# Optimization experiments

Hardware: AMD Instinct MI355X
Metric: run time of the kernel (lower is better)

Reference implementation:

```python
import jax, jax.numpy as jnp
import numpy as np
import math

N, B, S = 2048, 4, 1024
SFZ, IFZ, H, A = 384, 256, 8, 64
LN_EPS = 1e-5


def setup_inputs() -> dict:
    key = jax.random.key(0)
    ks = jax.random.split(key, 12)
    x = jax.random.normal(ks[0], (N, IFZ), dtype=jnp.float32)
    emb = jax.random.normal(ks[1], (B, S, SFZ), dtype=jnp.float32)
    mask = jax.random.randint(ks[2], (B, S), 0, 2).astype(bool)
    batch = jnp.sort(jax.random.randint(ks[3], (N,), 0, B)).astype(jnp.int64)
    sc = 1.0 / math.sqrt(IFZ)
    scs = 1.0 / math.sqrt(SFZ)
    Wq = jax.random.normal(ks[4], (IFZ, H * A), dtype=jnp.float32) * sc
    Wk = jax.random.normal(ks[5], (SFZ, H * A), dtype=jnp.float32) * scs
    Wv = jax.random.normal(ks[6], (SFZ, H * A), dtype=jnp.float32) * scs
    Wg = jax.random.normal(ks[7], (IFZ, H * A), dtype=jnp.float32) * sc
    bg = jnp.zeros((H * A,), dtype=jnp.float32)
    Wback = jax.random.normal(ks[8], (H * A, IFZ), dtype=jnp.float32) / math.sqrt(H * A)
    bback = jnp.zeros((IFZ,), dtype=jnp.float32)
    gamma = jnp.ones((IFZ,), dtype=jnp.float32)
    beta = jnp.zeros((IFZ,), dtype=jnp.float32)
    return {"x": x, "packed_sequence_emb": emb, "packed_sequence_mask": mask,
            "batch": batch, "Wq": Wq, "Wk": Wk, "Wv": Wv, "Wg": Wg, "bg": bg,
            "Wback": Wback, "bback": bback, "gamma": gamma, "beta": beta}


def _masked_softmax(scores, mask):
    # scores: [N,S,H], mask: [N,S,1] bool; softmax over S with padded entries zeroed
    neg = jnp.finfo(scores.dtype).min
    s = jnp.where(mask, scores, neg)
    s = s - jnp.max(s, axis=1, keepdims=True)
    e = jnp.exp(s) * mask
    return e / (jnp.sum(e, axis=1, keepdims=True) + 1e-9)


def reference(x, packed_sequence_emb, packed_sequence_mask, batch,
              Wq, Wk, Wv, Wg, bg, Wback, bback, gamma, beta):
    scale = math.sqrt(A)
    q = (x @ Wq).reshape(N, H, A)                               # [N,H,A]
    k = (packed_sequence_emb @ Wk).reshape(B, S, H, A)          # [B,S,H,A]
    v = (packed_sequence_emb @ Wv).reshape(B, S, H, A)
    # scores per (node, candidate-batch), then gather node's own batch entry;
    # avoids materializing k[batch] of shape [N,S,H,A]
    scores_all = jnp.einsum('nha,bsha->nbsh', q, k) / scale     # [N,B,S,H]
    idx = batch[:, None, None, None].astype(jnp.int32)
    scores = jnp.take_along_axis(scores_all, idx, axis=1)[:, 0]  # [N,S,H]
    bmask = packed_sequence_mask[batch][..., None]               # [N,S,1]
    w = _masked_softmax(scores, bmask)                           # [N,S,H]
    feat_all = jnp.einsum('nsh,bsha->nbha', w, v)                # [N,B,H,A]
    feat = jnp.take_along_axis(feat_all, idx, axis=1)[:, 0]      # [N,H,A]
    gate = jax.nn.sigmoid(x @ Wg + bg).reshape(N, H, A)
    new = (gate * feat).reshape(N, H * A) @ Wback + bback        # [N,IFZ]
    y = math.sqrt(2.0) * x + new
    mu = jnp.mean(y, axis=-1, keepdims=True)
    var = jnp.mean((y - mu) ** 2, axis=-1, keepdims=True)
    out = (y - mu) * jax.lax.rsqrt(var + LN_EPS) * gamma + beta
    seq_aa_logits = jnp.sum(scores[..., :2], axis=-1)            # [N,S]
    return out, seq_aa_logits
```

## Files before the change

### kernel.cpp

```cpp
#include <hip/hip_runtime.h>
#include <hip/hip_bf16.h>

#define NND 2048
#define BBATCH 4
#define SS 1024
#define SFZ 384
#define IFZ 256
#define HH 8
#define AA 64
#define HA 512
#define NBX 48
#define NSPL 8

typedef __attribute__((ext_vector_type(8))) short bf16x8;
typedef __attribute__((ext_vector_type(4))) float f32x4;
typedef __attribute__((ext_vector_type(2))) unsigned int u32x2;

__device__ __forceinline__ unsigned short f2bf(float f) {
    union { float f; unsigned u; } a; a.f = f;
    unsigned r = a.u + 0x7fffu + ((a.u >> 16) & 1u);
    return (unsigned short)(r >> 16);
}
__device__ __forceinline__ float bf2f(unsigned short u) {
    return __uint_as_float((unsigned)u << 16);
}

__device__ __forceinline__ bf16x8 cvt8(const float* __restrict__ p) {
    const float4 f0 = *(const float4*)p;
    const float4 f1 = *(const float4*)(p + 4);
    bf16x8 o;
    o[0] = (short)f2bf(f0.x); o[1] = (short)f2bf(f0.y);
    o[2] = (short)f2bf(f0.z); o[3] = (short)f2bf(f0.w);
    o[4] = (short)f2bf(f1.x); o[5] = (short)f2bf(f1.y);
    o[6] = (short)f2bf(f1.z); o[7] = (short)f2bf(f1.w);
    return o;
}

__device__ __forceinline__ bf16x8 gld16(const unsigned short* p) {
    bf16x8 r;
    asm volatile("global_load_dwordx4 %0, %1, off" : "=&v"(r) : "v"(p));
    return r;
}
__device__ __forceinline__ f32x4 gldf4(const float* p) {
    f32x4 r;
    asm volatile("global_load_dwordx4 %0, %1, off" : "=&v"(r) : "v"(p));
    return r;
}
__device__ __forceinline__ u32x2 gld8(const unsigned short* p) {
    u32x2 r;
    asm volatile("global_load_dwordx2 %0, %1, off" : "=&v"(r) : "v"(p));
    return r;
}
__device__ __forceinline__ float gldf(const float* p) {
    float r;
    asm volatile("global_load_dword %0, %1, off" : "=&v"(r) : "v"(p));
    return r;
}
#define VMWAIT0() do { \
    asm volatile("s_waitcnt vmcnt(0)" ::: "memory"); \
    __builtin_amdgcn_sched_barrier(0); \
} while (0)

__device__ __forceinline__ void tile_transpose(
    const float* __restrict__ src, unsigned short* __restrict__ dst,
    int K, int N, int kt, int nt, int t)
{
    __shared__ unsigned short tile[64][65];
    const int k0 = kt * 64, n0 = nt * 64;
    const int tr = t >> 6, tc = t & 63;
    #pragma unroll
    for (int r = 0; r < 16; ++r)
        tile[tr + r*4][tc] = f2bf(src[(size_t)(k0 + tr + r*4) * N + n0 + tc]);
    __syncthreads();
    #pragma unroll
    for (int r = 0; r < 16; ++r)
        dst[(size_t)(n0 + tr + r*4) * K + k0 + tc] = tile[tc][tr + r*4];
}

__global__ __launch_bounds__(256) void prep_kernel(
    const float* __restrict__ Wk, const float* __restrict__ Wv,
    const float* __restrict__ Wq, const float* __restrict__ Wg,
    const float* __restrict__ Wback,
    const void* __restrict__ mask_raw, const void* __restrict__ batch_raw,
    unsigned short* __restrict__ WkT, unsigned short* __restrict__ WvT,
    unsigned short* __restrict__ WqT, unsigned short* __restrict__ WgT,
    unsigned short* __restrict__ WbackT,
    float* __restrict__ mask_f, int* __restrict__ seg)
{
    const int bx = blockIdx.x, t = threadIdx.x;
    if (bx < 48)  { tile_transpose(Wk, WkT, SFZ, HA, bx/8, bx%8, t); return; }
    if (bx < 96)  { const int i = bx-48;  tile_transpose(Wv, WvT, SFZ, HA, i/8, i%8, t); return; }
    if (bx < 128) { const int i = bx-96;  tile_transpose(Wq, WqT, IFZ, HA, i/8, i%8, t); return; }
    if (bx < 160) { const int i = bx-128; tile_transpose(Wg, WgT, IFZ, HA, i/8, i%8, t); return; }
    if (bx < 192) { const int i = bx-160; tile_transpose(Wback, WbackT, HA, IFZ, i/4, i%4, t); return; }
    __shared__ int fl[4];
    __shared__ int fb;
    __shared__ int cnt[4];
    if (t < 4) { fl[t] = 0; cnt[t] = 0; }
    if (t == 0) fb = 0;
    __syncthreads();
    const unsigned char*  mb = (const unsigned char*)mask_raw;
    const unsigned short* mh = (const unsigned short*)mask_raw;
    const unsigned int*   mw = (const unsigned int*)mask_raw;
    int f0 = 0, f1 = 0, f2 = 0, f3 = 0;
    for (int i = t; i < 2048; i += 256) {
        unsigned short h = mh[i];
        if (h == 0x3f80u) f0 = 1;
        if ((i & 1) == 0 && h != 0) f1 = 1;
    }
    for (int i = t; i < 4096; i += 256)
        if ((i & 3) != 0 && mb[i] != 0) f2 = 1;
    for (int i = t; i < 1024; i += 256)
        if ((i & 1) != 0 && mw[i] != 0) f3 = 1;
    const int* bw = (const int*)batch_raw;
    int f4 = 0;
    for (int i = t + 1; i < 2048; i += 256)
        if (bw[i] < bw[i-1]) f4 = 1;
    if (f0) atomicOr(&fl[0], 1);
    if (f1) atomicOr(&fl[1], 1);
    if (f2) atomicOr(&fl[2], 1);
    if (f3) atomicOr(&fl[3], 1);
    if (f4) atomicOr(&fb, 1);
    __syncthreads();
    int mode;
    if (fl[0])      mode = fl[1] ? 1 : 0;
    else if (fl[2]) mode = 2;
    else if (fl[3]) mode = 3;
    else            mode = 4;
    for (int s = t; s < BBATCH*SS; s += 256) {
        int m;
        switch (mode) {
            case 0:  m = (mw[s]   != 0); break;
            case 1:  m = (mh[s]   != 0); break;
            case 2:  m = (mb[s]   != 0); break;
            case 3:  m = (mw[s]   != 0); break;
            default: m = (mw[2*s] != 0); break;
        }
        mask_f[s] = m ? 1.0f : 0.0f;
    }
    const int b64 = fb;
    for (int i = t; i < NND; i += 256) {
        const int bv = (b64 ? bw[2*i] : bw[i]) & 3;
        atomicAdd(&cnt[bv], 1);
    }
    __syncthreads();
    if (t == 0) {
        int s = 0;
        for (int b = 0; b < 4; ++b) { seg[2*b] = s; s += cnt[b]; seg[2*b+1] = s; }
    }
}

__global__ __launch_bounds__(256, 2) void proj_mfma(
    const float* __restrict__ emb, const float* __restrict__ x,
    const unsigned short* __restrict__ WkT, const unsigned short* __restrict__ WvT,
    const unsigned short* __restrict__ WqT, const unsigned short* __restrict__ WgT,
    const float* __restrict__ bg,
    unsigned short* __restrict__ k_blk, unsigned short* __restrict__ vT_bf,
    unsigned short* __restrict__ q_bf, float* __restrict__ gate_ws)
{
    __shared__ unsigned short v_l[16][520];
    const int t = threadIdx.x, w = t >> 6, lane = t & 63;
    const int m16 = lane & 15, quad = lane >> 4;
    const int bx = blockIdx.x;
    if (bx < 512) {
        const int r0 = (bx >> 1) * 16;
        const int b = r0 >> 10, srow = r0 & (SS - 1);
        const float* ap = emb + (size_t)(r0 + m16) * SFZ + quad * 8;
        bf16x8 af[12];
        #pragma unroll
        for (int j = 0; j < 12; ++j) af[j] = cvt8(ap + j * 32);
        const unsigned short* Wt = (bx & 1) ? WvT : WkT;
        #pragma unroll
        for (int g = 0; g < 2; ++g) {
            const int n0g = w * 128 + g * 64;
            const unsigned short* bp0 = Wt + (size_t)(n0g +  0 + m16) * SFZ + quad * 8;
            const unsigned short* bp1 = Wt + (size_t)(n0g + 16 + m16) * SFZ + quad * 8;
            const unsigned short* bp2 = Wt + (size_t)(n0g + 32 + m16) * SFZ + quad * 8;
            const unsigned short* bp3 = Wt + (size_t)(n0g + 48 + m16) * SFZ + quad * 8;
            f32x4 a0 = (f32x4){0.f, 0.f, 0.f, 0.f};
            f32x4 a1 = a0, a2 = a0, a3 = a0;
            bf16x8 wb[24];
            #pragma unroll
            for (int j = 0; j < 6; ++j) {
                wb[j*4+0] = gld16(bp0 + j * 32);
                wb[j*4+1] = gld16(bp1 + j * 32);
                wb[j*4+2] = gld16(bp2 + j * 32);
                wb[j*4+3] = gld16(bp3 + j * 32);
            }
            VMWAIT0();
            #pragma unroll
            for (int j = 0; j < 6; ++j) {
                a0 = __builtin_amdgcn_mfma_f32_16x16x32_bf16(af[j], wb[j*4+0], a0, 0, 0, 0);
                a1 = __builtin_amdgcn_mfma_f32_16x16x32_bf16(af[j], wb[j*4+1], a1, 0, 0, 0);
                a2 = __builtin_amdgcn_mfma_f32_16x16x32_bf16(af[j], wb[j*4+2], a2, 0, 0, 0);
                a3 = __builtin_amdgcn_mfma_f32_16x16x32_bf16(af[j], wb[j*4+3], a3, 0, 0, 0);
            }
            #pragma unroll
            for (int j = 6; j < 12; ++j) {
                wb[(j-6)*4+0] = gld16(bp0 + j * 32);
                wb[(j-6)*4+1] = gld16(bp1 + j * 32);
                wb[(j-6)*4+2] = gld16(bp2 + j * 32);
                wb[(j-6)*4+3] = gld16(bp3 + j * 32);
            }
            VMWAIT0();
            #pragma unroll
            for (int j = 6; j < 12; ++j) {
                a0 = __builtin_amdgcn_mfma_f32_16x16x32_bf16(af[j], wb[(j-6)*4+0], a0, 0, 0, 0);
                a1 = __builtin_amdgcn_mfma_f32_16x16x32_bf16(af[j], wb[(j-6)*4+1], a1, 0, 0, 0);
                a2 = __builtin_amdgcn_mfma_f32_16x16x32_bf16(af[j], wb[(j-6)*4+2], a2, 0, 0, 0);
                a3 = __builtin_amdgcn_mfma_f32_16x16x32_bf16(af[j], wb[(j-6)*4+3], a3, 0, 0, 0);
            }
            f32x4 dd[4] = {a0, a1, a2, a3};
            if ((bx & 1) == 0) {
                #pragma unroll
                for (int u = 0; u < 4; ++u) {
                    const int n0 = n0g + u * 16;
                    const int head = n0 >> 6, coff = (n0 & 63) + m16;
                    unsigned short* kb = k_blk + (((size_t)(b * HH + head)) * SS) * 64 + coff;
                    #pragma unroll
                    for (int r = 0; r < 4; ++r)
                        kb[(size_t)(srow + quad * 4 + r) * 64] = f2bf(dd[u][r]);
                }
            } else {
                #pragma unroll
                for (int u = 0; u < 4; ++u) {
                    const int c0 = n0g + u * 16 + m16;
                    #pragma unroll
                    for (int r = 0; r < 4; ++r)
                        v_l[quad * 4 + r][c0] = f2bf(dd[u][r]);
                }
            }
        }
        if (bx & 1) {
            __syncthreads();
            for (int c = t; c < HA; c += 256) {
                unsigned short tmp[16];
                #pragma unroll
                for (int s = 0; s < 16; ++s) tmp[s] = v_l[s][c];
                unsigned short* dst = vT_bf + ((size_t)b * HA + c) * SS + srow;
                *(uint4*)dst       = ((const uint4*)tmp)[0];
                *(uint4*)(dst + 8) = ((const uint4*)tmp)[1];
            }
        }
    } else {
        const int i = bx - 512;
        const int r0 = (i >> 2) * 16;
        const int tensor = (i & 3) >> 1, half = i & 1;
        const unsigned short* Wt = tensor ? WgT : WqT;
        const float* ap = x + (size_t)(r0 + m16) * IFZ + quad * 8;
        bf16x8 af[8];
        #pragma unroll
        for (int j = 0; j < 8; ++j) af[j] = cvt8(ap + j * 32);
        const int n0b = half * 256 + w * 64;
        const unsigned short* bp0 = Wt + (size_t)(n0b +  0 + m16) * IFZ + quad * 8;
        const unsigned short* bp1 = Wt + (size_t)(n0b + 16 + m16) * IFZ + quad * 8;
        const unsigned short* bp2 = Wt + (size_t)(n0b + 32 + m16) * IFZ + quad * 8;
        const unsigned short* bp3 = Wt + (size_t)(n0b + 48 + m16) * IFZ + quad * 8;
        bf16x8 wb[32];
        #pragma unroll
        for (int j = 0; j < 8; ++j) {
            wb[j*4+0] = gld16(bp0 + j * 32);
            wb[j*4+1] = gld16(bp1 + j * 32);
            wb[j*4+2] = gld16(bp2 + j * 32);
            wb[j*4+3] = gld16(bp3 + j * 32);
        }
        VMWAIT0();
        f32x4 a0 = (f32x4){0.f, 0.f, 0.f, 0.f};
        f32x4 a1 = a0, a2 = a0, a3 = a0;
        #pragma unroll
        for (int j = 0; j < 8; ++j) {
            a0 = __builtin_amdgcn_mfma_f32_16x16x32_bf16(af[j], wb[j*4+0], a0, 0, 0, 0);
            a1 = __builtin_amdgcn_mfma_f32_16x16x32_bf16(af[j], wb[j*4+1], a1, 0, 0, 0);
            a2 = __builtin_amdgcn_mfma_f32_16x16x32_bf16(af[j], wb[j*4+2], a2, 0, 0, 0);
            a3 = __builtin_amdgcn_mfma_f32_16x16x32_bf16(af[j], wb[j*4+3], a3, 0, 0, 0);
        }
        f32x4 dd[4] = {a0, a1, a2, a3};
        if (tensor == 0) {
            #pragma unroll
            for (int u = 0; u < 4; ++u) {
                const int n0 = n0b + u * 16;
                #pragma unroll
                for (int r = 0; r < 4; ++r)
                    q_bf[(size_t)(r0 + quad * 4 + r) * HA + n0 + m16] = f2bf(dd[u][r]);
            }
        } else {
            #pragma unroll
            for (int u = 0; u < 4; ++u) {
                const int n0 = n0b + u * 16;
                const float bgv = bg[n0 + m16];
                #pragma unroll
                for (int r = 0; r < 4; ++r)
                    gate_ws[(size_t)(r0 + quad * 4 + r) * HA + n0 + m16] =
                        1.f / (1.f + __expf(-(dd[u][r] + bgv)));
            }
        }
    }
}

__global__ __launch_bounds__(256, 2) void attn_kernel(
    const unsigned short* __restrict__ k_blk, const unsigned short* __restrict__ vT_bf,
    const unsigned short* __restrict__ q_bf, const float* __restrict__ mask_f,
    const int* __restrict__ seg, unsigned short* __restrict__ part_O,
    float2* __restrict__ part_ml, float* __restrict__ out_logits)
{
    __shared__ unsigned short P_lds[4][16][136];
    __shared__ float raw0[16][132];
    const int bid = blockIdx.x;
    const int xcd = bid & 7;
    const int b   = xcd >> 1;
    const int idx = (bid >> 3) * 2 + (xcd & 1);
    const int z    = idx & 15;
    const int xblk = idx >> 4;
    const int hz    = z >> 3;
    const int split = z & 7;
    const int n0 = seg[2*b] + xblk * 16;
    const int nend = seg[2*b + 1];
    if (n0 >= nend) return;
    const int nvalid = min(16, nend - n0);

    const int t = threadIdx.x;
    const int w = t >> 6, lane = t & 63;
    const int m16 = lane & 15, quad = lane >> 4;
    const int h = hz * 4 + w;
    const int s0 = split * 128;

    int nq = n0 + m16; if (nq >= nend) nq = nend - 1;
    const unsigned short* qp = q_bf + (size_t)nq * HA + h * AA + quad * 8;
    const unsigned short* kb = k_blk + ((size_t)(b * HH + h)) * SS * 64;
    const unsigned short* vb = vT_bf + ((size_t)b * HA + h * AA) * SS;
    unsigned short (*Pw)[136] = P_lds[w];

    const bf16x8 qa0 = gld16(qp);
    const bf16x8 qa1 = gld16(qp + 32);
    bf16x8 kf[16];
    #pragma unroll
    for (int st = 0; st < 8; ++st) {
        const unsigned short* kp = kb + (size_t)(s0 + st * 16 + m16) * 64 + quad * 8;
        kf[2*st]   = gld16(kp);
        kf[2*st+1] = gld16(kp + 32);
    }
    float msk[8];
    #pragma unroll
    for (int st = 0; st < 8; ++st)
        msk[st] = gldf(mask_f + b * SS + s0 + st * 16 + m16);
    VMWAIT0();

    f32x4 d[8];
    #pragma unroll
    for (int st = 0; st < 8; ++st) {
        f32x4 acc = (f32x4){0.f, 0.f, 0.f, 0.f};
        acc = __builtin_amdgcn_mfma_f32_16x16x32_bf16(qa0, kf[2*st],   acc, 0, 0, 0);
        acc = __builtin_amdgcn_mfma_f32_16x16x32_bf16(qa1, kf[2*st+1], acc, 0, 0, 0);
        #pragma unroll
        for (int r = 0; r < 4; ++r) acc[r] *= 0.125f;
        d[st] = acc;
    }

    bf16x8 vf[16];
    #pragma unroll
    for (int sub = 0; sub < 4; ++sub) {
        const unsigned short* vp0 = vb + (size_t)m16 * SS + s0 + sub * 32 + quad * 8;
        #pragma unroll
        for (int a = 0; a < 4; ++a)
            vf[sub*4+a] = gld16(vp0 + (size_t)(a * 16) * SS);
    }
    __builtin_amdgcn_sched_barrier(0);

    if (hz == 0) {
        if (w == 0) {
            #pragma unroll
            for (int st = 0; st < 8; ++st)
                #pragma unroll
                for (int r = 0; r < 4; ++r)
                    raw0[quad * 4 + r][st * 16 + m16] = d[st][r];
        }
        __syncthreads();
        if (w == 1) {
            #pragma unroll
            for (int st = 0; st < 8; ++st)
                #pragma unroll
                for (int r = 0; r < 4; ++r) {
                    const int row = quad * 4 + r;
                    if (row < nvalid)
                        out_logits[(size_t)(n0 + row) * SS + s0 + st * 16 + m16] =
                            raw0[row][st * 16 + m16] + d[st][r];
                }
        }
    }
    float m_s[4], l_s[4];
    #pragma unroll
    for (int r = 0; r < 4; ++r) {
        float mx = -3.0e38f;
        #pragma unroll
        for (int st = 0; st < 8; ++st)
            mx = (msk[st] > 0.5f) ? fmaxf(mx, d[st][r]) : mx;
        mx = fmaxf(mx, __shfl_xor(mx, 1));
        mx = fmaxf(mx, __shfl_xor(mx, 2));
        mx = fmaxf(mx, __shfl_xor(mx, 4));
        mx = fmaxf(mx, __shfl_xor(mx, 8));
        m_s[r] = mx;
        float cs = 0.f;
        #pragma unroll
        for (int st = 0; st < 8; ++st) {
            const float e = (msk[st] > 0.5f) ? __expf(d[st][r] - mx) : 0.f;
            d[st][r] = e;
            cs += e;
        }
        cs += __shfl_xor(cs, 1);
        cs += __shfl_xor(cs, 2);
        cs += __shfl_xor(cs, 4);
        cs += __shfl_xor(cs, 8);
        l_s[r] = cs;
    }
    #pragma unroll
    for (int st = 0; st < 8; ++st)
        #pragma unroll
        for (int r = 0; r < 4; ++r)
            Pw[quad * 4 + r][st * 16 + m16] = f2bf(d[st][r]);
    bf16x8 pa[4];
    #pragma unroll
    for (int sub = 0; sub < 4; ++sub)
        pa[sub] = *(const bf16x8*)&Pw[m16][sub * 32 + quad * 8];
    VMWAIT0();
    f32x4 facc[4];
    #pragma unroll
    for (int a = 0; a < 4; ++a) facc[a] = (f32x4){0.f, 0.f, 0.f, 0.f};
    #pragma unroll
    for (int sub = 0; sub < 4; ++sub) {
        #pragma unroll
        for (int a = 0; a < 4; ++a)
            facc[a] = __builtin_amdgcn_mfma_f32_16x16x32_bf16(pa[sub], vf[sub*4+a], facc[a], 0, 0, 0);
    }
    unsigned short* po = part_O + (size_t)split * NND * HA;
    #pragma unroll
    for (int a = 0; a < 4; ++a)
        #pragma unroll
        for (int r = 0; r < 4; ++r) {
            const int row = quad * 4 + r;
            if (row < nvalid)
                po[(size_t)(n0 + row) * HA + h * AA + a * 16 + m16] = f2bf(facc[a][r]);
        }
    if (m16 == 0) {
        #pragma unroll
        for (int r = 0; r < 4; ++r) {
            const int row = quad * 4 + r;
            if (row < nvalid)
                part_ml[(size_t)split * NND * HH + (size_t)(n0 + row) * HH + h] =
                    make_float2(m_s[r], l_s[r]);
        }
    }
}

__global__ __launch_bounds__(256, 2) void back_ln_fused(
    const unsigned short* __restrict__ part_O, const float2* __restrict__ part_ml,
    const float* __restrict__ gate_ws, const unsigned short* __restrict__ WbackT,
    const float* __restrict__ x, const float* __restrict__ bback,
    const float* __restrict__ gamma, const float* __restrict__ beta,
    float* __restrict__ out)
{
    __shared__ float coef[NSPL][8][8];
    __shared__ unsigned short gf_l[8][520];
    __shared__ float nl[8][260];
    const int t = threadIdx.x, w = t >> 6, lane = t & 63;
    const int m16 = lane & 15, quad = lane >> 4;
    const int r0 = blockIdx.x * 8;
    if (t < 64) {
        const int row = t >> 3, h = t & 7, n = r0 + row;
        float2 ml[NSPL];
        #pragma unroll
        for (int s = 0; s < NSPL; ++s)
            ml[s] = part_ml[(size_t)s * NND * HH + (size_t)n * HH + h];
        float M = -3.0e38f;
        #pragma unroll
        for (int s = 0; s < NSPL; ++s) M = fmaxf(M, ml[s].x);
        float L = 0.f;
        float e[NSPL];
        #pragma unroll
        for (int s = 0; s < NSPL; ++s) { e[s] = __expf(ml[s].x - M); L += ml[s].y * e[s]; }
        const float invL = 1.f / (L + 1e-9f);
        #pragma unroll
        for (int s = 0; s < NSPL; ++s) coef[s][row][h] = e[s] * invL;
    }
    u32x2 pvv[4][NSPL];
    f32x4 gv[4];
    #pragma unroll
    for (int it = 0; it < 4; ++it) {
        const int i = (t + it * 256) * 4;
        const int row = i >> 9, c = i & (HA - 1);
        const int n = r0 + row;
        #pragma unroll
        for (int s = 0; s < NSPL; ++s)
            pvv[it][s] = gld8(&part_O[(size_t)s * NND * HA + (size_t)n * HA + c]);
        gv[it] = gldf4(&gate_ws[(size_t)n * HA + c]);
    }
    __syncthreads();
    VMWAIT0();
    #pragma unroll
    for (int it = 0; it < 4; ++it) {
        const int i = (t + it * 256) * 4;
        const int row = i >> 9, c = i & (HA - 1), h = c >> 6;
        float4 o = make_float4(0.f, 0.f, 0.f, 0.f);
        #pragma unroll
        for (int s = 0; s < NSPL; ++s) {
            const float cf = coef[s][row][h];
            o.x = fmaf(bf2f((unsigned short)(pvv[it][s][0] & 0xffffu)), cf, o.x);
            o.y = fmaf(bf2f((unsigned short)(pvv[it][s][0] >> 16)),     cf, o.y);
            o.z = fmaf(bf2f((unsigned short)(pvv[it][s][1] & 0xffffu)), cf, o.z);
            o.w = fmaf(bf2f((unsigned short)(pvv[it][s][1] >> 16)),     cf, o.w);
        }
        ushort4 ob;
        ob.x = f2bf(gv[it][0] * o.x); ob.y = f2bf(gv[it][1] * o.y);
        ob.z = f2bf(gv[it][2] * o.z); ob.w = f2bf(gv[it][3] * o.w);
        *(ushort4*)&gf_l[row][c] = ob;
    }
    __syncthreads();
    bf16x8 af[16];
    #pragma unroll
    for (int j = 0; j < 16; ++j)
        af[j] = *(const bf16x8*)&gf_l[m16 & 7][quad * 8 + j * 32];
    const unsigned short* bq0 = WbackT + (size_t)(w * 64 +  0 + m16) * HA + quad * 8;
    const unsigned short* bq1 = WbackT + (size_t)(w * 64 + 16 + m16) * HA + quad * 8;
    const unsigned short* bq2 = WbackT + (size_t)(w * 64 + 32 + m16) * HA + quad * 8;
    const unsigned short* bq3 = WbackT + (size_t)(w * 64 + 48 + m16) * HA + quad * 8;
    f32x4 a0 = (f32x4){0.f, 0.f, 0.f, 0.f};
    f32x4 a1 = a0, a2 = a0, a3 = a0;
    #pragma unroll
    for (int jb = 0; jb < 4; ++jb) {
        bf16x8 wb[16];
        #pragma unroll
        for (int j = 0; j < 4; ++j) {
            wb[j*4+0] = gld16(bq0 + (jb*4 + j) * 32);
            wb[j*4+1] = gld16(bq1 + (jb*4 + j) * 32);
            wb[j*4+2] = gld16(bq2 + (jb*4 + j) * 32);
            wb[j*4+3] = gld16(bq3 + (jb*4 + j) * 32);
        }
        VMWAIT0();
        #pragma unroll
        for (int j = 0; j < 4; ++j) {
            a0 = __builtin_amdgcn_mfma_f32_16x16x32_bf16(af[jb*4+j], wb[j*4+0], a0, 0, 0, 0);
            a1 = __builtin_amdgcn_mfma_f32_16x16x32_bf16(af[jb*4+j], wb[j*4+1], a1, 0, 0, 0);
            a2 = __builtin_amdgcn_mfma_f32_16x16x32_bf16(af[jb*4+j], wb[j*4+2], a2, 0, 0, 0);
            a3 = __builtin_amdgcn_mfma_f32_16x16x32_bf16(af[jb*4+j], wb[j*4+3], a3, 0, 0, 0);
        }
    }
    {
        f32x4 dd[4] = {a0, a1, a2, a3};
        #pragma unroll
        for (int u = 0; u < 4; ++u) {
            const int n0 = w * 64 + u * 16;
            const float bb = bback[n0 + m16];
            #pragma unroll
            for (int r = 0; r < 4; ++r) {
                const int rr = quad * 4 + r;
                if (rr < 8) nl[rr][n0 + m16] = dd[u][r] + bb;
            }
        }
    }
    __syncthreads();
    const int row = t >> 5, li = t & 31;
    const float* xr = x + (size_t)(r0 + row) * IFZ;
    float yv[8];
    float s1 = 0.f, s2 = 0.f;
    #pragma unroll
    for (int j = 0; j < 8; ++j) {
        const int c = li + j * 32;
        const float v = fmaf(1.41421356237309515f, xr[c], nl[row][c]);
        yv[j] = v; s1 += v; s2 += v * v;
    }
    #pragma unroll
    for (int off = 16; off >= 1; off >>= 1) {
        s1 += __shfl_xor(s1, off);
        s2 += __shfl_xor(s2, off);
    }
    const float mu  = s1 * (1.f / IFZ);
    const float var = s2 * (1.f / IFZ) - mu * mu;
    const float rv  = rsqrtf(var + 1e-5f);
    float* orow = out + (size_t)(r0 + row) * IFZ;
    #pragma unroll
    for (int j = 0; j < 8; ++j) {
        const int c = li + j * 32;
        orow[c] = (yv[j] - mu) * rv * gamma[c] + beta[c];
    }
}

extern "C" void kernel_launch(void* const* d_in, const int* in_sizes, int n_in,
                              void* d_out, int out_size, void* d_ws, size_t ws_size,
                              hipStream_t stream) {
    const float* x     = (const float*)d_in[0];
    const float* emb   = (const float*)d_in[1];
    const void*  mraw  = d_in[2];
    const void*  braw  = d_in[3];
    const float* Wq    = (const float*)d_in[4];
    const float* Wk    = (const float*)d_in[5];
    const float* Wv    = (const float*)d_in[6];
    const float* Wg    = (const float*)d_in[7];
    const float* bg    = (const float*)d_in[8];
    const float* Wback = (const float*)d_in[9];
    const float* bback = (const float*)d_in[10];
    const float* gamma = (const float*)d_in[11];
    const float* beta  = (const float*)d_in[12];

    char* ws = (char*)d_ws;
    const size_t MB = 1048576;
    size_t off = 0;
    float*          mask_f  = (float*)(ws + off);  off += 16384;
    int*            seg     = (int*)(ws + off);    off += 16384;
    unsigned short* WkT     = (unsigned short*)(ws + off); off += 393216;
    unsigned short* WvT     = (unsigned short*)(ws + off); off += 393216;
    unsigned short* WqT     = (unsigned short*)(ws + off); off += 262144;
    unsigned short* WgT     = (unsigned short*)(ws + off); off += 262144;
    unsigned short* WbackT  = (unsigned short*)(ws + off); off += 262144;
    unsigned short* k_blk   = (unsigned short*)(ws + off); off += 4*MB;
    unsigned short* vT_bf   = (unsigned short*)(ws + off); off += 4*MB;
    unsigned short* q_bf    = (unsigned short*)(ws + off); off += 2*MB;
    float*          gate_ws = (float*)(ws + off); off += 4*MB;
    unsigned short* part_O  = (unsigned short*)(ws + off); off += 16*MB;
    float2*         part_ml = (float2*)(ws + off); off += 1*MB;

    float* out        = (float*)d_out;
    float* out_logits = out + (size_t)NND * IFZ;

    hipLaunchKernelGGL(prep_kernel, dim3(193), dim3(256), 0, stream,
                       Wk, Wv, Wq, Wg, Wback, mraw, braw,
                       WkT, WvT, WqT, WgT, WbackT, mask_f, seg);
    hipLaunchKernelGGL(proj_mfma, dim3(1024), dim3(256), 0, stream,
                       emb, x, WkT, WvT, WqT, WgT, bg, k_blk, vT_bf, q_bf, gate_ws);
    hipLaunchKernelGGL(attn_kernel, dim3(BBATCH * NBX * 16), dim3(256), 0, stream,
                       k_blk, vT_bf, q_bf, mask_f, seg, part_O, part_ml, out_logits);
    hipLaunchKernelGGL(back_ln_fused, dim3(NND / 8), dim3(256), 0, stream,
                       part_O, part_ml, gate_ws, WbackT, x, bback, gamma, beta, out);
}
```

Baseline: 204.1 us.

## Reuse K/V fragments across node groups in attention and merge projection blocks

The attention kernel now has each block loop over up to 8 groups of 16 nodes. K, V and the mask stay loaded in registers across those groups, and the next group's Q fragments are prefetched while the current one is computed. The grid shrinks from 3072 to 384 blocks. The projection kernel has each block compute both K and V (or both Q and gate) from a single conversion of the input rows, halving its grid. This cuts redundant global loads of K, V and the activations, at the cost of fewer blocks, less parallelism, and serialized per-block work with a barrier inside the loop.

```diff
diff --git a/kernel.cpp b/kernel.cpp
--- a/kernel.cpp
+++ b/kernel.cpp
@@ -9,7 +9,8 @@
 #define HH 8
 #define AA 64
 #define HA 512
-#define NBX 48
+#define ABLK 6
+#define NGRP 8
 #define NSPL 8
 
 typedef __attribute__((ext_vector_type(8))) short bf16x8;
@@ -162,136 +163,140 @@
     const int t = threadIdx.x, w = t >> 6, lane = t & 63;
     const int m16 = lane & 15, quad = lane >> 4;
     const int bx = blockIdx.x;
-    if (bx < 512) {
-        const int r0 = (bx >> 1) * 16;
+    if (bx < 256) {
+        const int r0 = bx * 16;
         const int b = r0 >> 10, srow = r0 & (SS - 1);
         const float* ap = emb + (size_t)(r0 + m16) * SFZ + quad * 8;
         bf16x8 af[12];
         #pragma unroll
         for (int j = 0; j < 12; ++j) af[j] = cvt8(ap + j * 32);
-        const unsigned short* Wt = (bx & 1) ? WvT : WkT;
-        #pragma unroll
-        for (int g = 0; g < 2; ++g) {
-            const int n0g = w * 128 + g * 64;
-            const unsigned short* bp0 = Wt + (size_t)(n0g +  0 + m16) * SFZ + quad * 8;
-            const unsigned short* bp1 = Wt + (size_t)(n0g + 16 + m16) * SFZ + quad * 8;
-            const unsigned short* bp2 = Wt + (size_t)(n0g + 32 + m16) * SFZ + quad * 8;
-            const unsigned short* bp3 = Wt + (size_t)(n0g + 48 + m16) * SFZ + quad * 8;
-            f32x4 a0 = (f32x4){0.f, 0.f, 0.f, 0.f};
-            f32x4 a1 = a0, a2 = a0, a3 = a0;
-            bf16x8 wb[24];
-            #pragma unroll
-            for (int j = 0; j < 6; ++j) {
+        #pragma unroll
+        for (int tensor = 0; tensor < 2; ++tensor) {
+            const unsigned short* Wt = tensor ? WvT : WkT;
+            #pragma unroll
+            for (int g = 0; g < 2; ++g) {
+                const int n0g = w * 128 + g * 64;
+                const unsigned short* bp0 = Wt + (size_t)(n0g +  0 + m16) * SFZ + quad * 8;
+                const unsigned short* bp1 = Wt + (size_t)(n0g + 16 + m16) * SFZ + quad * 8;
+                const unsigned short* bp2 = Wt + (size_t)(n0g + 32 + m16) * SFZ + quad * 8;
+                const unsigned short* bp3 = Wt + (size_t)(n0g + 48 + m16) * SFZ + quad * 8;
+                f32x4 a0 = (f32x4){0.f, 0.f, 0.f, 0.f};
+                f32x4 a1 = a0, a2 = a0, a3 = a0;
+                bf16x8 wb[24];
+                #pragma unroll
+                for (int j = 0; j < 6; ++j) {
+                    wb[j*4+0] = gld16(bp0 + j * 32);
+                    wb[j*4+1] = gld16(bp1 + j * 32);
+                    wb[j*4+2] = gld16(bp2 + j * 32);
+                    wb[j*4+3] = gld16(bp3 + j * 32);
+                }
+                VMWAIT0();
+                #pragma unroll
+                for (int j = 0; j < 6; ++j) {
+                    a0 = __builtin_amdgcn_mfma_f32_16x16x32_bf16(af[j], wb[j*4+0], a0, 0, 0, 0);
+                    a1 = __builtin_amdgcn_mfma_f32_16x16x32_bf16(af[j], wb[j*4+1], a1, 0, 0, 0);
+                    a2 = __builtin_amdgcn_mfma_f32_16x16x32_bf16(af[j], wb[j*4+2], a2, 0, 0, 0);
+                    a3 = __builtin_amdgcn_mfma_f32_16x16x32_bf16(af[j], wb[j*4+3], a3, 0, 0, 0);
+                }
+                #pragma unroll
+                for (int j = 6; j < 12; ++j) {
+                    wb[(j-6)*4+0] = gld16(bp0 + j * 32);
+                    wb[(j-6)*4+1] = gld16(bp1 + j * 32);
+                    wb[(j-6)*4+2] = gld16(bp2 + j * 32);
+                    wb[(j-6)*4+3] = gld16(bp3 + j * 32);
+                }
+                VMWAIT0();
+                #pragma unroll
+                for (int j = 6; j < 12; ++j) {
+                    a0 = __builtin_amdgcn_mfma_f32_16x16x32_bf16(af[j], wb[(j-6)*4+0], a0, 0, 0, 0);
+                    a1 = __builtin_amdgcn_mfma_f32_16x16x32_bf16(af[j], wb[(j-6)*4+1], a1, 0, 0, 0);
+                    a2 = __builtin_amdgcn_mfma_f32_16x16x32_bf16(af[j], wb[(j-6)*4+2], a2, 0, 0, 0);
+                    a3 = __builtin_amdgcn_mfma_f32_16x16x32_bf16(af[j], wb[(j-6)*4+3], a3, 0, 0, 0);
+                }
+                f32x4 dd[4] = {a0, a1, a2, a3};
+                if (tensor == 0) {
+                    #pragma unroll
+                    for (int u = 0; u < 4; ++u) {
+                        const int n0 = n0g + u * 16;
+                        const int head = n0 >> 6, coff = (n0 & 63) + m16;
+                        unsigned short* kb = k_blk + (((size_t)(b * HH + head)) * SS) * 64 + coff;
+                        #pragma unroll
+                        for (int r = 0; r < 4; ++r)
+                            kb[(size_t)(srow + quad * 4 + r) * 64] = f2bf(dd[u][r]);
+                    }
+                } else {
+                    #pragma unroll
+                    for (int u = 0; u < 4; ++u) {
+                        const int c0 = n0g + u * 16 + m16;
+                        #pragma unroll
+                        for (int r = 0; r < 4; ++r)
+                            v_l[quad * 4 + r][c0] = f2bf(dd[u][r]);
+                    }
+                }
+            }
+        }
+        __syncthreads();
+        for (int c = t; c < HA; c += 256) {
+            unsigned short tmp[16];
+            #pragma unroll
+            for (int s = 0; s < 16; ++s) tmp[s] = v_l[s][c];
+            unsigned short* dst = vT_bf + ((size_t)b * HA + c) * SS + srow;
+            *(uint4*)dst       = ((const uint4*)tmp)[0];
+            *(uint4*)(dst + 8) = ((const uint4*)tmp)[1];
+        }
+    } else {
+        const int i = bx - 256;
+        const int r0 = (i >> 1) * 16;
+        const int half = i & 1;
+        const float* ap = x + (size_t)(r0 + m16) * IFZ + quad * 8;
+        bf16x8 af[8];
+        #pragma unroll
+        for (int j = 0; j < 8; ++j) af[j] = cvt8(ap + j * 32);
+        const int n0b = half * 256 + w * 64;
+        #pragma unroll
+        for (int tensor = 0; tensor < 2; ++tensor) {
+            const unsigned short* Wt = tensor ? WgT : WqT;
+            const unsigned short* bp0 = Wt + (size_t)(n0b +  0 + m16) * IFZ + quad * 8;
+            const unsigned short* bp1 = Wt + (size_t)(n0b + 16 + m16) * IFZ + quad * 8;
+            const unsigned short* bp2 = Wt + (size_t)(n0b + 32 + m16) * IFZ + quad * 8;
+            const unsigned short* bp3 = Wt + (size_t)(n0b + 48 + m16) * IFZ + quad * 8;
+            bf16x8 wb[32];
+            #pragma unroll
+            for (int j = 0; j < 8; ++j) {
                 wb[j*4+0] = gld16(bp0 + j * 32);
                 wb[j*4+1] = gld16(bp1 + j * 32);
                 wb[j*4+2] = gld16(bp2 + j * 32);
                 wb[j*4+3] = gld16(bp3 + j * 32);
             }
             VMWAIT0();
-            #pragma unroll
-            for (int j = 0; j < 6; ++j) {
+            f32x4 a0 = (f32x4){0.f, 0.f, 0.f, 0.f};
+            f32x4 a1 = a0, a2 = a0, a3 = a0;
+            #pragma unroll
+            for (int j = 0; j < 8; ++j) {
                 a0 = __builtin_amdgcn_mfma_f32_16x16x32_bf16(af[j], wb[j*4+0], a0, 0, 0, 0);
                 a1 = __builtin_amdgcn_mfma_f32_16x16x32_bf16(af[j], wb[j*4+1], a1, 0, 0, 0);
                 a2 = __builtin_amdgcn_mfma_f32_16x16x32_bf16(af[j], wb[j*4+2], a2, 0, 0, 0);
                 a3 = __builtin_amdgcn_mfma_f32_16x16x32_bf16(af[j], wb[j*4+3], a3, 0, 0, 0);
             }
-            #pragma unroll
-            for (int j = 6; j < 12; ++j) {
-                wb[(j-6)*4+0] = gld16(bp0 + j * 32);
-                wb[(j-6)*4+1] = gld16(bp1 + j * 32);
-                wb[(j-6)*4+2] = gld16(bp2 + j * 32);
-                wb[(j-6)*4+3] = gld16(bp3 + j * 32);
-            }
-            VMWAIT0();
-            #pragma unroll
-            for (int j = 6; j < 12; ++j) {
-                a0 = __builtin_amdgcn_mfma_f32_16x16x32_bf16(af[j], wb[(j-6)*4+0], a0, 0, 0, 0);
-                a1 = __builtin_amdgcn_mfma_f32_16x16x32_bf16(af[j], wb[(j-6)*4+1], a1, 0, 0, 0);
-                a2 = __builtin_amdgcn_mfma_f32_16x16x32_bf16(af[j], wb[(j-6)*4+2], a2, 0, 0, 0);
-                a3 = __builtin_amdgcn_mfma_f32_16x16x32_bf16(af[j], wb[(j-6)*4+3], a3, 0, 0, 0);
-            }
             f32x4 dd[4] = {a0, a1, a2, a3};
-            if ((bx & 1) == 0) {
+            if (tensor == 0) {
                 #pragma unroll
                 for (int u = 0; u < 4; ++u) {
-                    const int n0 = n0g + u * 16;
-                    const int head = n0 >> 6, coff = (n0 & 63) + m16;
-                    unsigned short* kb = k_blk + (((size_t)(b * HH + head)) * SS) * 64 + coff;
+                    const int n0 = n0b + u * 16;
                     #pragma unroll
                     for (int r = 0; r < 4; ++r)
-                        kb[(size_t)(srow + quad * 4 + r) * 64] = f2bf(dd[u][r]);
+                        q_bf[(size_t)(r0 + quad * 4 + r) * HA + n0 + m16] = f2bf(dd[u][r]);
                 }
             } else {
                 #pragma unroll
                 for (int u = 0; u < 4; ++u) {
-                    const int c0 = n0g + u * 16 + m16;
+                    const int n0 = n0b + u * 16;
+                    const float bgv = bg[n0 + m16];
                     #pragma unroll
                     for (int r = 0; r < 4; ++r)
-                        v_l[quad * 4 + r][c0] = f2bf(dd[u][r]);
+                        gate_ws[(size_t)(r0 + quad * 4 + r) * HA + n0 + m16] =
+                            1.f / (1.f + __expf(-(dd[u][r] + bgv)));
                 }
-            }
-        }
-        if (bx & 1) {
-            __syncthreads();
-            for (int c = t; c < HA; c += 256) {
-                unsigned short tmp[16];
-                #pragma unroll
-                for (int s = 0; s < 16; ++s) tmp[s] = v_l[s][c];
-                unsigned short* dst = vT_bf + ((size_t)b * HA + c) * SS + srow;
-                *(uint4*)dst       = ((const uint4*)tmp)[0];
-                *(uint4*)(dst + 8) = ((const uint4*)tmp)[1];
-            }
-        }
-    } else {
-        const int i = bx - 512;
-        const int r0 = (i >> 2) * 16;
-        const int tensor = (i & 3) >> 1, half = i & 1;
-        const unsigned short* Wt = tensor ? WgT : WqT;
-        const float* ap = x + (size_t)(r0 + m16) * IFZ + quad * 8;
-        bf16x8 af[8];
-        #pragma unroll
-        for (int j = 0; j < 8; ++j) af[j] = cvt8(ap + j * 32);
-        const int n0b = half * 256 + w * 64;
-        const unsigned short* bp0 = Wt + (size_t)(n0b +  0 + m16) * IFZ + quad * 8;
-        const unsigned short* bp1 = Wt + (size_t)(n0b + 16 + m16) * IFZ + quad * 8;
-        const unsigned short* bp2 = Wt + (size_t)(n0b + 32 + m16) * IFZ + quad * 8;
-        const unsigned short* bp3 = Wt + (size_t)(n0b + 48 + m16) * IFZ + quad * 8;
-        bf16x8 wb[32];
-        #pragma unroll
-        for (int j = 0; j < 8; ++j) {
-            wb[j*4+0] = gld16(bp0 + j * 32);
-            wb[j*4+1] = gld16(bp1 + j * 32);
-            wb[j*4+2] = gld16(bp2 + j * 32);
-            wb[j*4+3] = gld16(bp3 + j * 32);
-        }
-        VMWAIT0();
-        f32x4 a0 = (f32x4){0.f, 0.f, 0.f, 0.f};
-        f32x4 a1 = a0, a2 = a0, a3 = a0;
-        #pragma unroll
-        for (int j = 0; j < 8; ++j) {
-            a0 = __builtin_amdgcn_mfma_f32_16x16x32_bf16(af[j], wb[j*4+0], a0, 0, 0, 0);
-            a1 = __builtin_amdgcn_mfma_f32_16x16x32_bf16(af[j], wb[j*4+1], a1, 0, 0, 0);
-            a2 = __builtin_amdgcn_mfma_f32_16x16x32_bf16(af[j], wb[j*4+2], a2, 0, 0, 0);
-            a3 = __builtin_amdgcn_mfma_f32_16x16x32_bf16(af[j], wb[j*4+3], a3, 0, 0, 0);
-        }
-        f32x4 dd[4] = {a0, a1, a2, a3};
-        if (tensor == 0) {
-            #pragma unroll
-            for (int u = 0; u < 4; ++u) {
-                const int n0 = n0b + u * 16;
-                #pragma unroll
-                for (int r = 0; r < 4; ++r)
-                    q_bf[(size_t)(r0 + quad * 4 + r) * HA + n0 + m16] = f2bf(dd[u][r]);
-            }
-        } else {
-            #pragma unroll
-            for (int u = 0; u < 4; ++u) {
-                const int n0 = n0b + u * 16;
-                const float bgv = bg[n0 + m16];
-                #pragma unroll
-                for (int r = 0; r < 4; ++r)
-                    gate_ws[(size_t)(r0 + quad * 4 + r) * HA + n0 + m16] =
-                        1.f / (1.f + __expf(-(dd[u][r] + bgv)));
             }
         }
     }
@@ -304,7 +309,7 @@
     float2* __restrict__ part_ml, float* __restrict__ out_logits)
 {
     __shared__ unsigned short P_lds[4][16][136];
-    __shared__ float raw0[16][132];
+    __shared__ float raw0[2][16][132];
     const int bid = blockIdx.x;
     const int xcd = bid & 7;
     const int b   = xcd >> 1;
@@ -313,10 +318,9 @@
     const int xblk = idx >> 4;
     const int hz    = z >> 3;
     const int split = z & 7;
-    const int n0 = seg[2*b] + xblk * 16;
-    const int nend = seg[2*b + 1];
-    if (n0 >= nend) return;
-    const int nvalid = min(16, nend - n0);
+    const int nbase = seg[2*b] + xblk * (16 * NGRP);
+    const int nend  = seg[2*b + 1];
+    if (nbase >= nend) return;
 
     const int t = threadIdx.x;
     const int w = t >> 6, lane = t & 63;
@@ -324,14 +328,11 @@
     const int h = hz * 4 + w;
     const int s0 = split * 128;
 
-    int nq = n0 + m16; if (nq >= nend) nq = nend - 1;
-    const unsigned short* qp = q_bf + (size_t)nq * HA + h * AA + quad * 8;
     const unsigned short* kb = k_blk + ((size_t)(b * HH + h)) * SS * 64;
     const unsigned short* vb = vT_bf + ((size_t)b * HA + h * AA) * SS;
+    const unsigned short* qbase = q_bf + (size_t)h * AA + quad * 8;
     unsigned short (*Pw)[136] = P_lds[w];
 
-    const bf16x8 qa0 = gld16(qp);
-    const bf16x8 qa1 = gld16(qp + 32);
     bf16x8 kf[16];
     #pragma unroll
     for (int st = 0; st < 8; ++st) {
@@ -339,114 +340,131 @@
         kf[2*st]   = gld16(kp);
         kf[2*st+1] = gld16(kp + 32);
     }
+    bf16x8 vf[16];
+    #pragma unroll
+    for (int sub = 0; sub < 4; ++sub) {
+        const unsigned short* vp0 = vb + (size_t)m16 * SS + s0 + sub * 32 + quad * 8;
+        #pragma unroll
+        for (int a = 0; a < 4; ++a)
+            vf[sub*4+a] = gld16(vp0 + (size_t)(a * 16) * SS);
+    }
     float msk[8];
     #pragma unroll
     for (int st = 0; st < 8; ++st)
         msk[st] = gldf(mask_f + b * SS + s0 + st * 16 + m16);
+    int nq0 = nbase + m16; if (nq0 >= nend) nq0 = nend - 1;
+    bf16x8 qc0 = gld16(qbase + (size_t)nq0 * HA);
+    bf16x8 qc1 = gld16(qbase + (size_t)nq0 * HA + 32);
     VMWAIT0();
 
-    f32x4 d[8];
-    #pragma unroll
-    for (int st = 0; st < 8; ++st) {
-        f32x4 acc = (f32x4){0.f, 0.f, 0.f, 0.f};
-        acc = __builtin_amdgcn_mfma_f32_16x16x32_bf16(qa0, kf[2*st],   acc, 0, 0, 0);
-        acc = __builtin_amdgcn_mfma_f32_16x16x32_bf16(qa1, kf[2*st+1], acc, 0, 0, 0);
-        #pragma unroll
-        for (int r = 0; r < 4; ++r) acc[r] *= 0.125f;
-        d[st] = acc;
-    }
-
-    bf16x8 vf[16];
-    #pragma unroll
-    for (int sub = 0; sub < 4; ++sub) {
-        const unsigned short* vp0 = vb + (size_t)m16 * SS + s0 + sub * 32 + quad * 8;
+    bf16x8 qn0 = qc0, qn1 = qc1;
+    for (int g = 0; g < NGRP; ++g) {
+        const int n0g = nbase + g * 16;
+        if (n0g >= nend) break;
+        if (g > 0) {
+            VMWAIT0();
+            qc0 = qn0; qc1 = qn1;
+        }
+        const int nvalid = min(16, nend - n0g);
+
+        f32x4 d[8];
+        #pragma unroll
+        for (int st = 0; st < 8; ++st) {
+            f32x4 acc = (f32x4){0.f, 0.f, 0.f, 0.f};
+            acc = __builtin_amdgcn_mfma_f32_16x16x32_bf16(qc0, kf[2*st],   acc, 0, 0, 0);
+            acc = __builtin_amdgcn_mfma_f32_16x16x32_bf16(qc1, kf[2*st+1], acc, 0, 0, 0);
+            #pragma unroll
+            for (int r = 0; r < 4; ++r) acc[r] *= 0.125f;
+            d[st] = acc;
+        }
+        if (g + 1 < NGRP && nbase + (g + 1) * 16 < nend) {
+            int nqn = nbase + (g + 1) * 16 + m16; if (nqn >= nend) nqn = nend - 1;
+            qn0 = gld16(qbase + (size_t)nqn * HA);
+            qn1 = gld16(qbase + (size_t)nqn * HA + 32);
+        }
+        __builtin_amdgcn_sched_barrier(0);
+
+        if (hz == 0) {
+            if (w == 0) {
+                #pragma unroll
+                for (int st = 0; st < 8; ++st)
+                    #pragma unroll
+                    for (int r = 0; r < 4; ++r)
+                        raw0[g & 1][quad * 4 + r][st * 16 + m16] = d[st][r];
+            }
+            __syncthreads();
+            if (w == 1) {
+                #pragma unroll
+                for (int st = 0; st < 8; ++st)
+                    #pragma unroll
+                    for (int r = 0; r < 4; ++r) {
+                        const int row = quad * 4 + r;
+                        if (row < nvalid)
+                            out_logits[(size_t)(n0g + row) * SS + s0 + st * 16 + m16] =
+                                raw0[g & 1][row][st * 16 + m16] + d[st][r];
+                    }
+            }
+        }
+        float m_s[4], l_s[4];
+        #pragma unroll
+        for (int r = 0; r < 4; ++r) {
+            float mx = -3.0e38f;
+            #pragma unroll
+            for (int st = 0; st < 8; ++st)
+                mx = (msk[st] > 0.5f) ? fmaxf(mx, d[st][r]) : mx;
+            mx = fmaxf(mx, __shfl_xor(mx, 1));
+            mx = fmaxf(mx, __shfl_xor(mx, 2));
+            mx = fmaxf(mx, __shfl_xor(mx, 4));
+            mx = fmaxf(mx, __shfl_xor(mx, 8));
+            m_s[r] = mx;
+            float cs = 0.f;
+            #pragma unroll
+            for (int st = 0; st < 8; ++st) {
+                const float e = (msk[st] > 0.5f) ? __expf(d[st][r] - mx) : 0.f;
+                d[st][r] = e;
+                cs += e;
+            }
+            cs += __shfl_xor(cs, 1);
+            cs += __shfl_xor(cs, 2);
+            cs += __shfl_xor(cs, 4);
+            cs += __shfl_xor(cs, 8);
+            l_s[r] = cs;
+        }
+        #pragma unroll
+        for (int st = 0; st < 8; ++st)
+            #pragma unroll
+            for (int r = 0; r < 4; ++r)
+                Pw[quad * 4 + r][st * 16 + m16] = f2bf(d[st][r]);
+        bf16x8 pa[4];
+        #pragma unroll
+        for (int sub = 0; sub < 4; ++sub)
+            pa[sub] = *(const bf16x8*)&Pw[m16][sub * 32 + quad * 8];
+        f32x4 facc[4];
+        #pragma unroll
+        for (int a = 0; a < 4; ++a) facc[a] = (f32x4){0.f, 0.f, 0.f, 0.f};
+        #pragma unroll
+        for (int sub = 0; sub < 4; ++sub) {
+            #pragma unroll
+            for (int a = 0; a < 4; ++a)
+                facc[a] = __builtin_amdgcn_mfma_f32_16x16x32_bf16(pa[sub], vf[sub*4+a], facc[a], 0, 0, 0);
+        }
+        unsigned short* po = part_O + (size_t)split * NND * HA;
         #pragma unroll
         for (int a = 0; a < 4; ++a)
-            vf[sub*4+a] = gld16(vp0 + (size_t)(a * 16) * SS);
-    }
-    __builtin_amdgcn_sched_barrier(0);
-
-    if (hz == 0) {
-        if (w == 0) {
-            #pragma unroll
-            for (int st = 0; st < 8; ++st)
-                #pragma unroll
-                for (int r = 0; r < 4; ++r)
-                    raw0[quad * 4 + r][st * 16 + m16] = d[st][r];
-        }
-        __syncthreads();
-        if (w == 1) {
-            #pragma unroll
-            for (int st = 0; st < 8; ++st)
-                #pragma unroll
-                for (int r = 0; r < 4; ++r) {
-                    const int row = quad * 4 + r;
-                    if (row < nvalid)
-                        out_logits[(size_t)(n0 + row) * SS + s0 + st * 16 + m16] =
-                            raw0[row][st * 16 + m16] + d[st][r];
-                }
-        }
-    }
-    float m_s[4], l_s[4];
-    #pragma unroll
-    for (int r = 0; r < 4; ++r) {
-        float mx = -3.0e38f;
-        #pragma unroll
-        for (int st = 0; st < 8; ++st)
-            mx = (msk[st] > 0.5f) ? fmaxf(mx, d[st][r]) : mx;
-        mx = fmaxf(mx, __shfl_xor(mx, 1));
-        mx = fmaxf(mx, __shfl_xor(mx, 2));
-        mx = fmaxf(mx, __shfl_xor(mx, 4));
-        mx = fmaxf(mx, __shfl_xor(mx, 8));
-        m_s[r] = mx;
-        float cs = 0.f;
-        #pragma unroll
-        for (int st = 0; st < 8; ++st) {
-            const float e = (msk[st] > 0.5f) ? __expf(d[st][r] - mx) : 0.f;
-            d[st][r] = e;
-            cs += e;
-        }
-        cs += __shfl_xor(cs, 1);
-        cs += __shfl_xor(cs, 2);
-        cs += __shfl_xor(cs, 4);
-        cs += __shfl_xor(cs, 8);
-        l_s[r] = cs;
-    }
-    #pragma unroll
-    for (int st = 0; st < 8; ++st)
-        #pragma unroll
-        for (int r = 0; r < 4; ++r)
-            Pw[quad * 4 + r][st * 16 + m16] = f2bf(d[st][r]);
-    bf16x8 pa[4];
-    #pragma unroll
-    for (int sub = 0; sub < 4; ++sub)
-        pa[sub] = *(const bf16x8*)&Pw[m16][sub * 32 + quad * 8];
-    VMWAIT0();
-    f32x4 facc[4];
-    #pragma unroll
-    for (int a = 0; a < 4; ++a) facc[a] = (f32x4){0.f, 0.f, 0.f, 0.f};
-    #pragma unroll
-    for (int sub = 0; sub < 4; ++sub) {
-        #pragma unroll
-        for (int a = 0; a < 4; ++a)
-            facc[a] = __builtin_amdgcn_mfma_f32_16x16x32_bf16(pa[sub], vf[sub*4+a], facc[a], 0, 0, 0);
-    }
-    unsigned short* po = part_O + (size_t)split * NND * HA;
-    #pragma unroll
-    for (int a = 0; a < 4; ++a)
-        #pragma unroll
-        for (int r = 0; r < 4; ++r) {
-            const int row = quad * 4 + r;
-            if (row < nvalid)
-                po[(size_t)(n0 + row) * HA + h * AA + a * 16 + m16] = f2bf(facc[a][r]);
-        }
-    if (m16 == 0) {
-        #pragma unroll
-        for (int r = 0; r < 4; ++r) {
-            const int row = quad * 4 + r;
-            if (row < nvalid)
-                part_ml[(size_t)split * NND * HH + (size_t)(n0 + row) * HH + h] =
-                    make_float2(m_s[r], l_s[r]);
+            #pragma unroll
+            for (int r = 0; r < 4; ++r) {
+                const int row = quad * 4 + r;
+                if (row < nvalid)
+                    po[(size_t)(n0g + row) * HA + h * AA + a * 16 + m16] = f2bf(facc[a][r]);
+            }
+        if (m16 == 0) {
+            #pragma unroll
+            for (int r = 0; r < 4; ++r) {
+                const int row = quad * 4 + r;
+                if (row < nvalid)
+                    part_ml[(size_t)split * NND * HH + (size_t)(n0g + row) * HH + h] =
+                        make_float2(m_s[r], l_s[r]);
+            }
         }
     }
 }
@@ -623,9 +641,9 @@
     hipLaunchKernelGGL(prep_kernel, dim3(193), dim3(256), 0, stream,
                        Wk, Wv, Wq, Wg, Wback, mraw, braw,
                        WkT, WvT, WqT, WgT, WbackT, mask_f, seg);
-    hipLaunchKernelGGL(proj_mfma, dim3(1024), dim3(256), 0, stream,
+    hipLaunchKernelGGL(proj_mfma, dim3(512), dim3(256), 0, stream,
                        emb, x, WkT, WvT, WqT, WgT, bg, k_blk, vT_bf, q_bf, gate_ws);
-    hipLaunchKernelGGL(attn_kernel, dim3(BBATCH * NBX * 16), dim3(256), 0, stream,
+    hipLaunchKernelGGL(attn_kernel, dim3(BBATCH * ABLK * 16), dim3(256), 0, stream,
                        k_blk, vT_bf, q_bf, mask_f, seg, part_O, part_ml, out_logits);
     hipLaunchKernelGGL(back_ln_fused, dim3(NND / 8), dim3(256), 0, stream,
                        part_O, part_ml, gate_ws, WbackT, x, bback, gamma, beta, out);
```

Measured after the change: 189.2 us. -7.3%, faster.
